# Performance work log

Hardware: AMD Instinct MI355X
Metric: run time of the kernel (lower is better)

The kernel has to match this reference:

```python
import jax, jax.numpy as jnp
import numpy as np

V, D, S, L, H, R, W = 32000, 512, 1536, 4, 4, 32, 128
HFF = int(2.0 * D)
N = S + 1          # anchor node at index 0 + S tokens
K = W + 2          # anchor edge + (W+1) causal window edges
LN_EPS = 1e-5


def _layer_norm(x, g, b):
    m = jnp.mean(x, axis=-1, keepdims=True)
    v = jnp.mean((x - m) ** 2, axis=-1, keepdims=True)
    return (x - m) * jax.lax.rsqrt(v + LN_EPS) * g + b


def _neighbors():
    # windowed causal neighborhood: node i sees nodes i-W..i, plus anchor (node 0)
    pos = jnp.arange(N)
    offs = jnp.arange(-W, 1)                     # W+1 offsets
    idx_w = pos[:, None] + offs[None, :]         # [N, W+1]
    valid_w = idx_w >= 0
    idx_w = jnp.maximum(idx_w, 0)
    anchor_valid = (pos > W)[:, None]            # avoid double-counting anchor when already in window
    idx = jnp.concatenate([jnp.zeros((N, 1), idx_w.dtype), idx_w], axis=1)   # [N, K]
    mask = jnp.concatenate([anchor_valid, valid_w], axis=1)                  # [N, K]
    return idx, mask


def setup_inputs() -> dict:
    key = jax.random.key(0)
    ks = jax.random.split(key, 10)
    std = 0.02
    return {
        'input_ids': jax.random.randint(ks[0], (1, S), 0, V),
        'embed': jax.random.normal(ks[1], (V, D), jnp.float32) * std,
        'pos_emb': jax.random.normal(ks[2], (S, D), jnp.float32) * std,
        'ln_in_g': jnp.ones((D,), jnp.float32),
        'ln_in_b': jnp.zeros((D,), jnp.float32),
        'anchor_state': jnp.zeros((), jnp.float32),
        'anchor_val': jax.random.normal(ks[3], (D,), jnp.float32) * std,
        'state_w': jax.random.normal(ks[4], (D,), jnp.float32) * std,
        'state_b': jnp.zeros((), jnp.float32),
        'wq': jax.random.normal(ks[5], (L, H, D, R), jnp.float32) * std,
        'wk': jax.random.normal(ks[6], (L, H, D, R), jnp.float32) * std,
        'gate': jnp.full((L,), 0.1, jnp.float32),
        'ln_g': jnp.ones((L, D), jnp.float32),
        'ln_b': jnp.zeros((L, D), jnp.float32),
        'ffn_w1': jax.random.normal(ks[7], (L, D, HFF), jnp.float32) * std,
        'ffn_b1': jnp.zeros((L, HFF), jnp.float32),
        'ffn_w2': jax.random.normal(ks[8], (L, HFF, D), jnp.float32) * std,
        'ffn_b2': jnp.zeros((L, D), jnp.float32),
        'ln2_g': jnp.ones((L, D), jnp.float32),
        'ln2_b': jnp.zeros((L, D), jnp.float32),
    }


def reference(input_ids, embed, pos_emb, ln_in_g, ln_in_b, anchor_state, anchor_val,
              state_w, state_b, wq, wk, gate, ln_g, ln_b,
              ffn_w1, ffn_b1, ffn_w2, ffn_b2, ln2_g, ln2_b):
    B = input_ids.shape[0]
    # token embedding + learned position encoding + input norm
    tok = embed[input_ids] + pos_emb[None]                 # [B,S,D]
    tok = _layer_norm(tok, ln_in_g, ln_in_b)
    tok_state = tok @ state_w + state_b                    # [B,S] scalar state per node
    # prepend anchor node
    val = jnp.concatenate([jnp.broadcast_to(anchor_val, (B, 1, D)), tok], axis=1)       # [B,N,D]
    state = jnp.concatenate([jnp.broadcast_to(anchor_state, (B, 1)), tok_state], axis=1)  # [B,N]
    idx, mask = _neighbors()
    scale = 1.0 / np.sqrt(R)
    for l in range(L):
        # low-rank multi-head pairwise scores on windowed neighborhood
        q = jnp.einsum('bnd,hdr->bnhr', val, wq[l])
        k = jnp.einsum('bnd,hdr->bnhr', val, wk[l])
        kg = k[:, idx]                                     # [B,N,K,H,R] gather
        s = jnp.einsum('bnhr,bnkhr->bnkh', q, kg) * scale  # [B,N,K,H]
        # signed_smoothmax head aggregation
        hw = jax.nn.softmax(jnp.abs(s), axis=-1)
        a = jnp.sum(s * hw, axis=-1)                       # [B,N,K]
        # signed_abs_softmax edge compression over neighborhood
        absa = jnp.where(mask[None], jnp.abs(a), -jnp.inf)
        e = jnp.sign(a) * jax.nn.softmax(absa, axis=-1)    # masked entries -> 0 weight
        # state-weighted edges
        sg = state[:, idx]                                 # [B,N,K]
        e = e * sg
        val_g = val[:, idx]                                # [B,N,K,D]
        d_val = jnp.einsum('bnk,bnkd->bnd', e, val_g)
        d_state = jnp.sum(e, axis=-1)
        # gated residual + post-norm
        state = state + gate[l] * d_state
        val = val + gate[l] * d_val
        val = _layer_norm(val, ln_g[l], ln_b[l])
        # value feed-forward (pre-norm, residual scale 1.0)
        h = jax.nn.gelu(_layer_norm(val, ln2_g[l], ln2_b[l]) @ ffn_w1[l] + ffn_b1[l], approximate=False)
        val = val + h @ ffn_w2[l] + ffn_b2[l]
    return val
```

## Files before the change

### kernel.cpp

```cpp
#include <hip/hip_runtime.h>
#include <hip/hip_bf16.h>

namespace {

constexpr int D    = 512;
constexpr int S    = 1536;
constexpr int N    = S + 1;
constexpr int L    = 4;
constexpr int H    = 4;
constexpr int R    = 32;
constexpr int W    = 128;
constexpr int HFF  = 1024;
constexpr float EPS = 1e-5f;

constexpr int TB   = 4;
constexpr int NB4  = (N + TB - 1) / TB;
constexpr int SP   = 133;
constexpr int SPAD = 136;

typedef __attribute__((ext_vector_type(8))) short short8;
typedef __attribute__((ext_vector_type(4))) float floatx4;

__device__ inline ushort f2bf(float x){
  __hip_bfloat16 h = __float2bfloat16(x);
  return *reinterpret_cast<ushort*>(&h);
}
__device__ inline float bf2f(uint u){
  union { uint u; float f; } c; c.u = u << 16; return c.f;
}

__device__ inline float wave_sum(float v){
#pragma unroll
  for (int o = 32; o; o >>= 1) v += __shfl_xor(v, o, 64);
  return v;
}
__device__ inline float wave_max(float v){
#pragma unroll
  for (int o = 32; o; o >>= 1) v = fmaxf(v, __shfl_xor(v, o, 64));
  return v;
}
__device__ inline float block_sum(float v, float* scr){
  v = wave_sum(v);
  __syncthreads();
  if ((threadIdx.x & 63) == 0) scr[threadIdx.x >> 6] = v;
  __syncthreads();
  return scr[0] + scr[1] + scr[2] + scr[3];
}

__global__ __launch_bounds__(256) void pack_wqk_bf(const float* __restrict__ wq,
                                                   const float* __restrict__ wk,
                                                   ushort* __restrict__ out){
  int i = blockIdx.x * 256 + threadIdx.x;
  int d = i & 511;
  int c = (i >> 9) & 255;
  int l = i >> 17;
  int cc = c & 127;
  int h = cc >> 5, r = cc & 31;
  const float* src = (c < 128) ? wq : wk;
  out[i] = f2bf(src[((l * H + h) * D + d) * R + r]);
}

__global__ __launch_bounds__(256) void transpose_bf(const float* __restrict__ src,
                                                    ushort* __restrict__ dst,
                                                    int rows, int cols){
  __shared__ float tile[32][33];
  const float* s = src + (size_t)blockIdx.z * rows * cols;
  ushort* d = dst + (size_t)blockIdx.z * rows * cols;
  int c0 = blockIdx.x * 32, r0 = blockIdx.y * 32;
  int tx = threadIdx.x & 31, ty = threadIdx.x >> 5;
  for (int rr = ty; rr < 32; rr += 8)
    tile[rr][tx] = s[(size_t)(r0 + rr) * cols + c0 + tx];
  __syncthreads();
  for (int rr = ty; rr < 32; rr += 8)
    d[(size_t)(c0 + rr) * rows + r0 + tx] = f2bf(tile[tx][rr]);
}

__global__ __launch_bounds__(256) void embed_ln_kernel(
    const int* __restrict__ ids, const float* __restrict__ embed,
    const float* __restrict__ pos, const float* __restrict__ g,
    const float* __restrict__ b, const float* __restrict__ anchor_val,
    const float* __restrict__ anchor_state, const float* __restrict__ state_w,
    const float* __restrict__ state_b, float* __restrict__ val,
    ushort* __restrict__ valbf, float* __restrict__ state)
{
  __shared__ float scr[4];
  int n = blockIdx.x, t = threadIdx.x;
  if (n == 0){
    float a0 = anchor_val[t], a1 = anchor_val[t + 256];
    val[t] = a0; val[t + 256] = a1;
    valbf[t] = f2bf(a0); valbf[t + 256] = f2bf(a1);
    if (t == 0) state[0] = anchor_state[0];
    return;
  }
  int tp = n - 1;
  int id = ids[tp];
  float x0 = embed[(size_t)id * D + t]       + pos[tp * D + t];
  float x1 = embed[(size_t)id * D + t + 256] + pos[tp * D + t + 256];
  float mean = block_sum(x0 + x1, scr) * (1.f / D);
  float var  = block_sum(x0 * x0 + x1 * x1, scr) * (1.f / D) - mean * mean;
  float rs   = rsqrtf(var + EPS);
  float y0 = (x0 - mean) * rs * g[t]       + b[t];
  float y1 = (x1 - mean) * rs * g[t + 256] + b[t + 256];
  val[n * D + t]       = y0;
  val[n * D + t + 256] = y1;
  valbf[n * D + t]       = f2bf(y0);
  valbf[n * D + t + 256] = f2bf(y1);
  float ts = block_sum(y0 * state_w[t] + y1 * state_w[t + 256], scr);
  if (t == 0) state[n] = ts + state_b[0];
}

template<int ACT>
__global__ __launch_bounds__(256) void gemm_bf16(
    const ushort* __restrict__ A, const ushort* __restrict__ Bt,
    const float* __restrict__ bias, const float* __restrict__ resid,
    float* __restrict__ C, ushort* __restrict__ Cbf,
    int M, int Kd, int Nc)
{
  constexpr int SLAB = 272;
  __shared__ ushort As[8 * SLAB];
  __shared__ ushort Bs[8 * SLAB];
  int row0 = blockIdx.y * 32;
  int col0 = blockIdx.x * 32;
  int t = threadIdx.x;
  int lane = t & 63, w = t >> 6;
  int wr = w & 1, wc = w >> 1;
  int q = lane >> 4, lm = lane & 15;

  int srow = t >> 3, skb = t & 7;
  int arow = min(row0 + srow, M - 1);
  const ushort* ag = A  + (size_t)arow * Kd + skb * 8;
  const ushort* bg = Bt + (size_t)(col0 + srow) * Kd + skb * 8;
  ushort* as = &As[skb * SLAB + srow * 8];
  ushort* bs = &Bs[skb * SLAB + srow * 8];

  const ushort* ar = &As[(wr * 16 + lm) * 8];
  const ushort* br = &Bs[(wc * 16 + lm) * 8];

  floatx4 acc = {0.f, 0.f, 0.f, 0.f};

  for (int k0 = 0; k0 < Kd; k0 += 64){
    uint4 av = *(const uint4*)(ag + k0);
    uint4 bv = *(const uint4*)(bg + k0);
    *(uint4*)as = av;
    *(uint4*)bs = bv;
    __syncthreads();
#pragma unroll
    for (int kk = 0; kk < 2; ++kk){
      short8 a = *(const short8*)(ar + (kk * 4 + q) * SLAB);
      short8 b = *(const short8*)(br + (kk * 4 + q) * SLAB);
      acc = __builtin_amdgcn_mfma_f32_16x16x32_bf16(a, b, acc, 0, 0, 0);
    }
    __syncthreads();
  }

  int col = col0 + wc * 16 + lm;
#pragma unroll
  for (int r = 0; r < 4; ++r){
    int row = row0 + wr * 16 + q * 4 + r;
    if (row >= M) continue;
    float v = acc[r] + (bias ? bias[col] : 0.f);
    if (ACT == 1) v = 0.5f * v * (1.f + erff(v * 0.70710678118654752f));
    if (resid) v += resid[(size_t)row * Nc + col];
    size_t o = (size_t)row * Nc + col;
    if (C)   C[o] = v;
    if (Cbf) Cbf[o] = f2bf(v);
  }
}

__global__ __launch_bounds__(256) void attn4_kernel(
    const ushort* __restrict__ qkbf, const float* __restrict__ val0,
    const ushort* __restrict__ val0bf, const float* __restrict__ state_in,
    float* __restrict__ val1, ushort* __restrict__ x2bf,
    float* __restrict__ state_out,
    const float* __restrict__ gate_p, const float* __restrict__ lng,
    const float* __restrict__ lnb, const float* __restrict__ ln2g,
    const float* __restrict__ ln2b)
{
  __shared__ float kg[64 * SPAD];
  __shared__ float qsh[TB * 128];
  __shared__ float ssh[16 * SPAD];
  __shared__ float ash[TB * SPAD];
  const int n0 = blockIdx.x * TB;
  const int t = threadIdx.x;
  const int w = t >> 6, l = t & 63;
  const float gate = gate_p[0];
  const float scale = 0.17677669529663687f;

#pragma unroll
  for (int i = t; i < TB * 128; i += 256){
    int it = i >> 7, ch = i & 127;
    int gr = min(n0 + it, N - 1);
    qsh[i] = bf2f((uint)qkbf[(size_t)gr * 256 + ch]);
  }

  for (int half = 0; half < 2; ++half){
    for (int i = t; i < SP * 16; i += 256){
      int c = i >> 4, c4 = i & 15;
      int g = (c == 132) ? 0 : min(max(n0 - W + c, 0), N - 1);
      uint2 v = *(const uint2*)&qkbf[(size_t)g * 256 + 128 + half * 64 + c4 * 4];
      int ch = c4 * 4;
      kg[(ch + 0) * SPAD + c] = bf2f(v.x & 0xffffu);
      kg[(ch + 1) * SPAD + c] = bf2f(v.x >> 16);
      kg[(ch + 2) * SPAD + c] = bf2f(v.y & 0xffffu);
      kg[(ch + 3) * SPAD + c] = bf2f(v.y >> 16);
    }
    __syncthreads();
    for (int tk = t; tk < TB * 2 * SP; tk += 256){
      int c = tk % SP;
      int th = tk / SP;
      int tok = th & 3, hh = th >> 2;
      int h = half * 2 + hh;
      const float* qs = &qsh[tok * 128 + h * 32];
      const float* ks = &kg[hh * 32 * SPAD + c];
      float acc = 0.f;
#pragma unroll
      for (int r = 0; r < 32; ++r) acc += qs[r] * ks[r * SPAD];
      ssh[(tok * 4 + h) * SPAD + c] = acc * scale;
    }
    __syncthreads();
  }

  for (int i = t; i < TB * SP; i += 256){
    int tok = i / SP, c = i - tok * SP;
    const float* sr = &ssh[tok * 4 * SPAD + c];
    float s0 = sr[0], s1 = sr[SPAD], s2 = sr[2 * SPAD], s3 = sr[3 * SPAD];
    float a0 = fabsf(s0), a1 = fabsf(s1), a2 = fabsf(s2), a3 = fabsf(s3);
    float m = fmaxf(fmaxf(a0, a1), fmaxf(a2, a3));
    float w0 = expf(a0 - m), w1 = expf(a1 - m), w2 = expf(a2 - m), w3 = expf(a3 - m);
    ash[tok * SPAD + c] = (s0 * w0 + s1 * w1 + s2 * w2 + s3 * w3) / (w0 + w1 + w2 + w3);
  }
  __syncthreads();

  {
    const int n = n0 + w;
    float* arow = &ash[w * SPAD];
    float a0 = arow[l];
    float a1 = arow[64 + l];
    float a2 = (l < 5) ? arow[128 + l] : 0.f;
    bool ok0 = (l >= w) && (n0 - W + l >= 0);
    bool ok1 = (n0 - W + 64 + l >= 0);
    bool ok2;
    if (l < 4)       ok2 = (l <= w);
    else if (l == 4) ok2 = (n > W);
    else             ok2 = false;
    float cand = -3.4e38f;
    if (ok0) cand = fabsf(a0);
    if (ok1) cand = fmaxf(cand, fabsf(a1));
    if (ok2) cand = fmaxf(cand, fabsf(a2));
    float m = wave_max(cand);
    float e0 = ok0 ? expf(fabsf(a0) - m) : 0.f;
    float e1 = ok1 ? expf(fabsf(a1) - m) : 0.f;
    float e2 = ok2 ? expf(fabsf(a2) - m) : 0.f;
    float inv = 1.f / wave_sum(e0 + e1 + e2);
    int g0 = min(max(n0 - W + l, 0), N - 1);
    int g1 = min(max(n0 - W + 64 + l, 0), N - 1);
    int g2 = (l < 4) ? min(n0 + l, N - 1) : 0;
    float sg0 = (a0 > 0.f) ? 1.f : ((a0 < 0.f) ? -1.f : 0.f);
    float sg1 = (a1 > 0.f) ? 1.f : ((a1 < 0.f) ? -1.f : 0.f);
    float sg2 = (a2 > 0.f) ? 1.f : ((a2 < 0.f) ? -1.f : 0.f);
    float t0 = sg0 * e0 * inv * state_in[g0];
    float t1 = sg1 * e1 * inv * state_in[g1];
    float t2 = (l < 5) ? sg2 * e2 * inv * state_in[g2] : 0.f;
    arow[l] = t0;
    arow[64 + l] = t1;
    if (l < 5) arow[128 + l] = t2;
    float ds = wave_sum(t0 + t1 + t2);
    if (l == 0 && n < N) state_out[n] = state_in[n] + gate * ds;
  }
  __syncthreads();

  float acc[TB][2];
#pragma unroll
  for (int k = 0; k < TB; ++k){ acc[k][0] = 0.f; acc[k][1] = 0.f; }
  {
    const int d0 = 2 * t;
    for (int c = 0; c < SP; ++c){
      int g = (c == 132) ? 0 : min(max(n0 - W + c, 0), N - 1);
      uint v = *(const uint*)&val0bf[(size_t)g * D + d0];
      float vx = bf2f(v & 0xffffu), vy = bf2f(v >> 16);
#pragma unroll
      for (int k = 0; k < TB; ++k){
        float e = ash[k * SPAD + c];
        acc[k][0] += e * vx;
        acc[k][1] += e * vy;
      }
    }
  }
  float* xbuf = kg;
  {
    const int d0 = 2 * t;
#pragma unroll
    for (int k = 0; k < TB; ++k){
      int nc = min(n0 + k, N - 1);
      float2 vv = *(const float2*)&val0[(size_t)nc * D + d0];
      xbuf[k * 520 + d0]     = vv.x + gate * acc[k][0];
      xbuf[k * 520 + d0 + 1] = vv.y + gate * acc[k][1];
    }
  }
  __syncthreads();

  {
    const int n = n0 + w;
    const int d = l * 8;
    const float* xr = &xbuf[w * 520 + d];
    float x[8];
#pragma unroll
    for (int j = 0; j < 8; ++j) x[j] = xr[j];
    float s1 = 0.f, s2 = 0.f;
#pragma unroll
    for (int j = 0; j < 8; ++j){ s1 += x[j]; s2 += x[j] * x[j]; }
    s1 = wave_sum(s1); s2 = wave_sum(s2);
    float mean = s1 * (1.f / D);
    float var  = s2 * (1.f / D) - mean * mean;
    float rs   = rsqrtf(var + EPS);
    float y[8];
    float u1 = 0.f, u2 = 0.f;
#pragma unroll
    for (int j = 0; j < 8; ++j){
      float yv = (x[j] - mean) * rs * lng[d + j] + lnb[d + j];
      y[j] = yv; u1 += yv; u2 += yv * yv;
    }
    u1 = wave_sum(u1); u2 = wave_sum(u2);
    float mean2 = u1 * (1.f / D);
    float var2  = u2 * (1.f / D) - mean2 * mean2;
    float rs2   = rsqrtf(var2 + EPS);
    if (n < N){
      *(float4*)&val1[(size_t)n * D + d]     = make_float4(y[0], y[1], y[2], y[3]);
      *(float4*)&val1[(size_t)n * D + d + 4] = make_float4(y[4], y[5], y[6], y[7]);
      uint4 pk;
      uint z0 = f2bf((y[0] - mean2) * rs2 * ln2g[d + 0] + ln2b[d + 0]);
      uint z1 = f2bf((y[1] - mean2) * rs2 * ln2g[d + 1] + ln2b[d + 1]);
      uint z2 = f2bf((y[2] - mean2) * rs2 * ln2g[d + 2] + ln2b[d + 2]);
      uint z3 = f2bf((y[3] - mean2) * rs2 * ln2g[d + 3] + ln2b[d + 3]);
      uint z4 = f2bf((y[4] - mean2) * rs2 * ln2g[d + 4] + ln2b[d + 4]);
      uint z5 = f2bf((y[5] - mean2) * rs2 * ln2g[d + 5] + ln2b[d + 5]);
      uint z6 = f2bf((y[6] - mean2) * rs2 * ln2g[d + 6] + ln2b[d + 6]);
      uint z7 = f2bf((y[7] - mean2) * rs2 * ln2g[d + 7] + ln2b[d + 7]);
      pk.x = z0 | (z1 << 16); pk.y = z2 | (z3 << 16);
      pk.z = z4 | (z5 << 16); pk.w = z6 | (z7 << 16);
      *(uint4*)&x2bf[(size_t)n * D + d] = pk;
    }
  }
}

}

extern "C" void kernel_launch(void* const* d_in, const int* in_sizes, int n_in,
                              void* d_out, int out_size, void* d_ws, size_t ws_size,
                              hipStream_t stream)
{
  (void)in_sizes; (void)n_in; (void)out_size; (void)ws_size;
  const int*   ids          = (const int*)d_in[0];
  const float* embed        = (const float*)d_in[1];
  const float* pos_emb      = (const float*)d_in[2];
  const float* ln_in_g      = (const float*)d_in[3];
  const float* ln_in_b      = (const float*)d_in[4];
  const float* anchor_state = (const float*)d_in[5];
  const float* anchor_val   = (const float*)d_in[6];
  const float* state_w      = (const float*)d_in[7];
  const float* state_b      = (const float*)d_in[8];
  const float* wq           = (const float*)d_in[9];
  const float* wk           = (const float*)d_in[10];
  const float* gate         = (const float*)d_in[11];
  const float* ln_g         = (const float*)d_in[12];
  const float* ln_b         = (const float*)d_in[13];
  const float* ffn_w1       = (const float*)d_in[14];
  const float* ffn_b1       = (const float*)d_in[15];
  const float* ffn_w2       = (const float*)d_in[16];
  const float* ffn_b2       = (const float*)d_in[17];
  const float* ln2_g        = (const float*)d_in[18];
  const float* ln2_b        = (const float*)d_in[19];
  float* out = (float*)d_out;

  float* wsf  = (float*)d_ws;
  float* val0 = wsf;  wsf += (size_t)N * D;
  float* val1 = wsf;  wsf += (size_t)N * D;
  ushort* wsu   = (ushort*)wsf;
  ushort* val0bf = wsu;  wsu += (size_t)N * D;
  ushort* x2bf   = wsu;  wsu += (size_t)N * D;
  ushort* hbf    = wsu;  wsu += (size_t)N * HFF;
  ushort* qkbf   = wsu;  wsu += (size_t)N * 256;
  ushort* wqkbf  = wsu;  wsu += (size_t)L * 256 * D;
  ushort* w1t    = wsu;  wsu += (size_t)L * HFF * D;
  ushort* w2t    = wsu;  wsu += (size_t)L * HFF * D;
  float* st0 = (float*)wsu;
  float* st1 = st0 + N;

  pack_wqk_bf<<<L * 512, 256, 0, stream>>>(wq, wk, wqkbf);
  transpose_bf<<<dim3(HFF / 32, D / 32, L), 256, 0, stream>>>(ffn_w1, w1t, D, HFF);
  transpose_bf<<<dim3(D / 32, HFF / 32, L), 256, 0, stream>>>(ffn_w2, w2t, HFF, D);
  embed_ln_kernel<<<N, 256, 0, stream>>>(ids, embed, pos_emb, ln_in_g, ln_in_b,
                                         anchor_val, anchor_state, state_w,
                                         state_b, val0, val0bf, st0);

  float* sin_  = st0;
  float* sout_ = st1;
  const int MT32 = (N + 31) / 32;
  for (int l = 0; l < L; ++l){
    gemm_bf16<0><<<dim3(256 / 32, MT32), 256, 0, stream>>>(
        val0bf, wqkbf + (size_t)l * 256 * D, nullptr, nullptr,
        nullptr, qkbf, N, D, 256);
    attn4_kernel<<<NB4, 256, 0, stream>>>(qkbf, val0, val0bf, sin_, val1, x2bf,
                                          sout_, gate + l, ln_g + l * D,
                                          ln_b + l * D, ln2_g + l * D,
                                          ln2_b + l * D);
    gemm_bf16<1><<<dim3(HFF / 32, MT32), 256, 0, stream>>>(
        x2bf, w1t + (size_t)l * HFF * D, ffn_b1 + l * HFF, nullptr,
        nullptr, hbf, N, D, HFF);
    float* dst = (l == L - 1) ? out : val0;
    gemm_bf16<0><<<dim3(D / 32, MT32), 256, 0, stream>>>(
        hbf, w2t + (size_t)l * HFF * D, ffn_b2 + l * D, val1,
        dst, val0bf, N, HFF, D);
    float* tmp = sin_; sin_ = sout_; sout_ = tmp;
  }
}
```

Measured before the change: 370.7 us.

## Merge all stages into one persistent kernel with software grid barriers

All separate launches (weight pack, transposes, embedding, and the per-layer GEMMs and attention) are replaced by a single persistent kernel of 512 blocks. Each stage loops over its tiles grid-stride, and stages are separated by a hierarchical atomic grid barrier. The aim is to remove launch overhead and inter-kernel gaps across about 19 launches. In exchange it adds barrier spin cost and relies on all 512 blocks being co-resident, which could deadlock or time out if occupancy falls short, and it limits tile parallelism to 512 blocks per stage.

```diff
diff --git a/kernel.cpp b/kernel.cpp
--- a/kernel.cpp
+++ b/kernel.cpp
@@ -1,5 +1,6 @@
 #include <hip/hip_runtime.h>
 #include <hip/hip_bf16.h>
+#include <stdint.h>
 
 namespace {
 
@@ -18,6 +19,11 @@
 constexpr int SP   = 133;
 constexpr int SPAD = 136;
 
+constexpr int GS   = 512;
+constexpr int SLAB = 272;
+
+constexpr int SM_BYTES = (64 * SPAD + TB * 128 + 16 * SPAD + TB * SPAD) * 4;
+
 typedef __attribute__((ext_vector_type(8))) short short8;
 typedef __attribute__((ext_vector_type(4))) float floatx4;
 
@@ -47,140 +53,184 @@
   return scr[0] + scr[1] + scr[2] + scr[3];
 }
 
-__global__ __launch_bounds__(256) void pack_wqk_bf(const float* __restrict__ wq,
-                                                   const float* __restrict__ wk,
-                                                   ushort* __restrict__ out){
-  int i = blockIdx.x * 256 + threadIdx.x;
-  int d = i & 511;
-  int c = (i >> 9) & 255;
-  int l = i >> 17;
-  int cc = c & 127;
-  int h = cc >> 5, r = cc & 31;
-  const float* src = (c < 128) ? wq : wk;
-  out[i] = f2bf(src[((l * H + h) * D + d) * R + r]);
-}
-
-__global__ __launch_bounds__(256) void transpose_bf(const float* __restrict__ src,
-                                                    ushort* __restrict__ dst,
-                                                    int rows, int cols){
-  __shared__ float tile[32][33];
-  const float* s = src + (size_t)blockIdx.z * rows * cols;
-  ushort* d = dst + (size_t)blockIdx.z * rows * cols;
-  int c0 = blockIdx.x * 32, r0 = blockIdx.y * 32;
-  int tx = threadIdx.x & 31, ty = threadIdx.x >> 5;
-  for (int rr = ty; rr < 32; rr += 8)
-    tile[rr][tx] = s[(size_t)(r0 + rr) * cols + c0 + tx];
-  __syncthreads();
-  for (int rr = ty; rr < 32; rr += 8)
-    d[(size_t)(c0 + rr) * rows + r0 + tx] = f2bf(tile[tx][rr]);
-}
-
-__global__ __launch_bounds__(256) void embed_ln_kernel(
+__device__ inline void grid_bar(uint* bar, uint gen){
+  __syncthreads();
+  if (threadIdx.x == 0){
+    __threadfence();
+    uint* slot = bar + ((blockIdx.x & 15) << 4);
+    uint prev = __hip_atomic_fetch_add(slot, 1u, __ATOMIC_ACQ_REL,
+                                       __HIP_MEMORY_SCOPE_AGENT);
+    if (prev + 1u == gen * (uint)(GS / 16)){
+      __hip_atomic_fetch_add(bar + 256, 1u, __ATOMIC_ACQ_REL,
+                             __HIP_MEMORY_SCOPE_AGENT);
+    }
+    const uint tgt = gen * 16u;
+    for (long it = 0; it < 10000000L; ++it){
+      if (__hip_atomic_load(bar + 256, __ATOMIC_RELAXED,
+                            __HIP_MEMORY_SCOPE_AGENT) >= tgt) break;
+      __builtin_amdgcn_s_sleep(1);
+    }
+    __threadfence();
+  }
+  __syncthreads();
+}
+
+static __device__ __forceinline__ void embed_phase(
     const int* __restrict__ ids, const float* __restrict__ embed,
     const float* __restrict__ pos, const float* __restrict__ g,
     const float* __restrict__ b, const float* __restrict__ anchor_val,
     const float* __restrict__ anchor_state, const float* __restrict__ state_w,
     const float* __restrict__ state_b, float* __restrict__ val,
-    ushort* __restrict__ valbf, float* __restrict__ state)
-{
-  __shared__ float scr[4];
-  int n = blockIdx.x, t = threadIdx.x;
-  if (n == 0){
-    float a0 = anchor_val[t], a1 = anchor_val[t + 256];
-    val[t] = a0; val[t + 256] = a1;
-    valbf[t] = f2bf(a0); valbf[t + 256] = f2bf(a1);
-    if (t == 0) state[0] = anchor_state[0];
-    return;
-  }
-  int tp = n - 1;
-  int id = ids[tp];
-  float x0 = embed[(size_t)id * D + t]       + pos[tp * D + t];
-  float x1 = embed[(size_t)id * D + t + 256] + pos[tp * D + t + 256];
-  float mean = block_sum(x0 + x1, scr) * (1.f / D);
-  float var  = block_sum(x0 * x0 + x1 * x1, scr) * (1.f / D) - mean * mean;
-  float rs   = rsqrtf(var + EPS);
-  float y0 = (x0 - mean) * rs * g[t]       + b[t];
-  float y1 = (x1 - mean) * rs * g[t + 256] + b[t + 256];
-  val[n * D + t]       = y0;
-  val[n * D + t + 256] = y1;
-  valbf[n * D + t]       = f2bf(y0);
-  valbf[n * D + t + 256] = f2bf(y1);
-  float ts = block_sum(y0 * state_w[t] + y1 * state_w[t + 256], scr);
-  if (t == 0) state[n] = ts + state_b[0];
+    ushort* __restrict__ valbf, float* __restrict__ state, char* SMbase)
+{
+  float* scr = (float*)SMbase;
+  const int t = threadIdx.x;
+  for (int n = blockIdx.x; n < N; n += GS){
+    if (n == 0){
+      float a0 = anchor_val[t], a1 = anchor_val[t + 256];
+      val[t] = a0; val[t + 256] = a1;
+      valbf[t] = f2bf(a0); valbf[t + 256] = f2bf(a1);
+      if (t == 0) state[0] = anchor_state[0];
+      continue;
+    }
+    int tp = n - 1;
+    int id = ids[tp];
+    float x0 = embed[(size_t)id * D + t]       + pos[tp * D + t];
+    float x1 = embed[(size_t)id * D + t + 256] + pos[tp * D + t + 256];
+    float mean = block_sum(x0 + x1, scr) * (1.f / D);
+    float var  = block_sum(x0 * x0 + x1 * x1, scr) * (1.f / D) - mean * mean;
+    float rs   = rsqrtf(var + EPS);
+    float y0 = (x0 - mean) * rs * g[t]       + b[t];
+    float y1 = (x1 - mean) * rs * g[t + 256] + b[t + 256];
+    val[n * D + t]       = y0;
+    val[n * D + t + 256] = y1;
+    valbf[n * D + t]       = f2bf(y0);
+    valbf[n * D + t + 256] = f2bf(y1);
+    float ts = block_sum(y0 * state_w[t] + y1 * state_w[t + 256], scr);
+    if (t == 0) state[n] = ts + state_b[0];
+  }
+}
+
+static __device__ __forceinline__ void pack_phase(
+    const float* __restrict__ wq, const float* __restrict__ wk,
+    ushort* __restrict__ out)
+{
+  for (int i = blockIdx.x * 256 + threadIdx.x; i < L * 256 * D; i += GS * 256){
+    int d = i & 511;
+    int c = (i >> 9) & 255;
+    int l = i >> 17;
+    int cc = c & 127;
+    int h = cc >> 5, r = cc & 31;
+    const float* src = (c < 128) ? wq : wk;
+    out[i] = f2bf(src[((l * H + h) * D + d) * R + r]);
+  }
+}
+
+static __device__ __forceinline__ void transpose_phase(
+    const float* __restrict__ ffn_w1, const float* __restrict__ ffn_w2,
+    ushort* __restrict__ w1t, ushort* __restrict__ w2t, char* SMbase)
+{
+  float* tile = (float*)SMbase;
+  const int t = threadIdx.x;
+  const int tx = t & 31, ty = t >> 5;
+  for (int tl = blockIdx.x; tl < 2 * L * 512; tl += GS){
+    const float* s; ushort* dd; int rows, cols, c0, r0;
+    if (tl < 2048){
+      int ll = tl >> 9, i = tl & 511;
+      rows = D; cols = HFF;
+      s  = ffn_w1 + (size_t)ll * D * HFF;
+      dd = w1t   + (size_t)ll * D * HFF;
+      c0 = (i & 31) << 5; r0 = (i >> 5) << 5;
+    } else {
+      int tl2 = tl - 2048;
+      int ll = tl2 >> 9, i = tl2 & 511;
+      rows = HFF; cols = D;
+      s  = ffn_w2 + (size_t)ll * D * HFF;
+      dd = w2t   + (size_t)ll * D * HFF;
+      c0 = (i & 15) << 5; r0 = (i >> 4) << 5;
+    }
+    __syncthreads();
+    for (int rr = ty; rr < 32; rr += 8)
+      tile[rr * 33 + tx] = s[(size_t)(r0 + rr) * cols + c0 + tx];
+    __syncthreads();
+    for (int rr = ty; rr < 32; rr += 8)
+      dd[(size_t)(c0 + rr) * rows + r0 + tx] = f2bf(tile[tx * 33 + rr]);
+  }
 }
 
 template<int ACT>
-__global__ __launch_bounds__(256) void gemm_bf16(
+static __device__ __forceinline__ void gemm_phase(
     const ushort* __restrict__ A, const ushort* __restrict__ Bt,
     const float* __restrict__ bias, const float* __restrict__ resid,
     float* __restrict__ C, ushort* __restrict__ Cbf,
-    int M, int Kd, int Nc)
-{
-  constexpr int SLAB = 272;
-  __shared__ ushort As[8 * SLAB];
-  __shared__ ushort Bs[8 * SLAB];
-  int row0 = blockIdx.y * 32;
-  int col0 = blockIdx.x * 32;
-  int t = threadIdx.x;
-  int lane = t & 63, w = t >> 6;
-  int wr = w & 1, wc = w >> 1;
-  int q = lane >> 4, lm = lane & 15;
-
-  int srow = t >> 3, skb = t & 7;
-  int arow = min(row0 + srow, M - 1);
-  const ushort* ag = A  + (size_t)arow * Kd + skb * 8;
-  const ushort* bg = Bt + (size_t)(col0 + srow) * Kd + skb * 8;
-  ushort* as = &As[skb * SLAB + srow * 8];
-  ushort* bs = &Bs[skb * SLAB + srow * 8];
-
-  const ushort* ar = &As[(wr * 16 + lm) * 8];
-  const ushort* br = &Bs[(wc * 16 + lm) * 8];
-
-  floatx4 acc = {0.f, 0.f, 0.f, 0.f};
-
-  for (int k0 = 0; k0 < Kd; k0 += 64){
-    uint4 av = *(const uint4*)(ag + k0);
-    uint4 bv = *(const uint4*)(bg + k0);
-    *(uint4*)as = av;
-    *(uint4*)bs = bv;
-    __syncthreads();
-#pragma unroll
-    for (int kk = 0; kk < 2; ++kk){
-      short8 a = *(const short8*)(ar + (kk * 4 + q) * SLAB);
-      short8 b = *(const short8*)(br + (kk * 4 + q) * SLAB);
-      acc = __builtin_amdgcn_mfma_f32_16x16x32_bf16(a, b, acc, 0, 0, 0);
-    }
-    __syncthreads();
-  }
-
-  int col = col0 + wc * 16 + lm;
-#pragma unroll
-  for (int r = 0; r < 4; ++r){
-    int row = row0 + wr * 16 + q * 4 + r;
-    if (row >= M) continue;
-    float v = acc[r] + (bias ? bias[col] : 0.f);
-    if (ACT == 1) v = 0.5f * v * (1.f + erff(v * 0.70710678118654752f));
-    if (resid) v += resid[(size_t)row * Nc + col];
-    size_t o = (size_t)row * Nc + col;
-    if (C)   C[o] = v;
-    if (Cbf) Cbf[o] = f2bf(v);
-  }
-}
-
-__global__ __launch_bounds__(256) void attn4_kernel(
-    const ushort* __restrict__ qkbf, const float* __restrict__ val0,
+    int M, int Kd, int Nc, char* SMbase)
+{
+  ushort* As = (ushort*)SMbase;
+  ushort* Bs = As + 8 * SLAB;
+  const int t = threadIdx.x;
+  const int lane = t & 63, w = t >> 6;
+  const int wr = w & 1, wc = w >> 1;
+  const int q = lane >> 4, lm = lane & 15;
+  const int srow = t >> 3, skb = t & 7;
+  const int ntx = Nc >> 5, nty = (M + 31) >> 5;
+  const int ntot = ntx * nty;
+
+  for (int tile = blockIdx.x; tile < ntot; tile += GS){
+    int row0 = (tile / ntx) << 5;
+    int col0 = (tile % ntx) << 5;
+    int arow = min(row0 + srow, M - 1);
+    const ushort* ag = A  + (size_t)arow * Kd + skb * 8;
+    const ushort* bg = Bt + (size_t)(col0 + srow) * Kd + skb * 8;
+    ushort* as = &As[skb * SLAB + srow * 8];
+    ushort* bs = &Bs[skb * SLAB + srow * 8];
+    const ushort* ar = &As[(wr * 16 + lm) * 8];
+    const ushort* br = &Bs[(wc * 16 + lm) * 8];
+
+    floatx4 acc = {0.f, 0.f, 0.f, 0.f};
+    for (int k0 = 0; k0 < Kd; k0 += 64){
+      uint4 av = *(const uint4*)(ag + k0);
+      uint4 bv = *(const uint4*)(bg + k0);
+      *(uint4*)as = av;
+      *(uint4*)bs = bv;
+      __syncthreads();
+#pragma unroll
+      for (int kk = 0; kk < 2; ++kk){
+        short8 a = *(const short8*)(ar + (kk * 4 + q) * SLAB);
+        short8 b = *(const short8*)(br + (kk * 4 + q) * SLAB);
+        acc = __builtin_amdgcn_mfma_f32_16x16x32_bf16(a, b, acc, 0, 0, 0);
+      }
+      __syncthreads();
+    }
+
+    int col = col0 + wc * 16 + lm;
+#pragma unroll
+    for (int r = 0; r < 4; ++r){
+      int row = row0 + wr * 16 + q * 4 + r;
+      if (row >= M) continue;
+      float v = acc[r] + (bias ? bias[col] : 0.f);
+      if (ACT == 1) v = 0.5f * v * (1.f + erff(v * 0.70710678118654752f));
+      if (resid) v += resid[(size_t)row * Nc + col];
+      size_t o = (size_t)row * Nc + col;
+      if (C)   C[o] = v;
+      if (Cbf) Cbf[o] = f2bf(v);
+    }
+  }
+}
+
+static __device__ __forceinline__ void attn_phase(
+    int blk, const ushort* __restrict__ qkbf, const float* __restrict__ val0,
     const ushort* __restrict__ val0bf, const float* __restrict__ state_in,
     float* __restrict__ val1, ushort* __restrict__ x2bf,
-    float* __restrict__ state_out,
-    const float* __restrict__ gate_p, const float* __restrict__ lng,
-    const float* __restrict__ lnb, const float* __restrict__ ln2g,
-    const float* __restrict__ ln2b)
-{
-  __shared__ float kg[64 * SPAD];
-  __shared__ float qsh[TB * 128];
-  __shared__ float ssh[16 * SPAD];
-  __shared__ float ash[TB * SPAD];
-  const int n0 = blockIdx.x * TB;
+    float* __restrict__ state_out, const float* __restrict__ gate_p,
+    const float* __restrict__ lng, const float* __restrict__ lnb,
+    const float* __restrict__ ln2g, const float* __restrict__ ln2b,
+    char* SMbase)
+{
+  float* kg  = (float*)SMbase;
+  float* qsh = kg + 64 * SPAD;
+  float* ssh = qsh + TB * 128;
+  float* ash = ssh + 16 * SPAD;
+  const int n0 = blk * TB;
   const int t = threadIdx.x;
   const int w = t >> 6, l = t & 63;
   const float gate = gate_p[0];
@@ -343,6 +393,63 @@
   }
 }
 
+__global__ void init_bar_kernel(uint* bar){
+  bar[threadIdx.x] = 0u;
+}
+
+__global__ __launch_bounds__(256, 2) void mega_kernel(
+    const int* __restrict__ ids, const float* __restrict__ embed,
+    const float* __restrict__ pos_emb, const float* __restrict__ ln_in_g,
+    const float* __restrict__ ln_in_b, const float* __restrict__ anchor_state,
+    const float* __restrict__ anchor_val, const float* __restrict__ state_w,
+    const float* __restrict__ state_b, const float* __restrict__ wq,
+    const float* __restrict__ wk, const float* __restrict__ gate,
+    const float* __restrict__ ln_g, const float* __restrict__ ln_b,
+    const float* __restrict__ ffn_w1, const float* __restrict__ ffn_b1,
+    const float* __restrict__ ffn_w2, const float* __restrict__ ffn_b2,
+    const float* __restrict__ ln2_g, const float* __restrict__ ln2_b,
+    float* __restrict__ out,
+    float* __restrict__ val0, float* __restrict__ val1,
+    ushort* __restrict__ val0bf, ushort* __restrict__ x2bf,
+    ushort* __restrict__ hbf, ushort* __restrict__ qkbf,
+    ushort* __restrict__ wqkbf, ushort* __restrict__ w1t,
+    ushort* __restrict__ w2t, float* __restrict__ st0,
+    float* __restrict__ st1, uint* __restrict__ bar)
+{
+  __shared__ __align__(16) char SM[SM_BYTES];
+  uint gen = 0;
+
+  embed_phase(ids, embed, pos_emb, ln_in_g, ln_in_b, anchor_val, anchor_state,
+              state_w, state_b, val0, val0bf, st0, SM);
+  pack_phase(wq, wk, wqkbf);
+  transpose_phase(ffn_w1, ffn_w2, w1t, w2t, SM);
+  grid_bar(bar, ++gen);
+
+  float* sin_  = st0;
+  float* sout_ = st1;
+  for (int l = 0; l < L; ++l){
+    gemm_phase<0>(val0bf, wqkbf + (size_t)l * 256 * D, nullptr, nullptr,
+                  nullptr, qkbf, N, D, 256, SM);
+    grid_bar(bar, ++gen);
+
+    for (int blk = blockIdx.x; blk < NB4; blk += GS)
+      attn_phase(blk, qkbf, val0, val0bf, sin_, val1, x2bf, sout_, gate + l,
+                 ln_g + l * D, ln_b + l * D, ln2_g + l * D, ln2_b + l * D, SM);
+    grid_bar(bar, ++gen);
+
+    gemm_phase<1>(x2bf, w1t + (size_t)l * HFF * D, ffn_b1 + l * HFF, nullptr,
+                  nullptr, hbf, N, D, HFF, SM);
+    grid_bar(bar, ++gen);
+
+    float* dst = (l == L - 1) ? out : val0;
+    gemm_phase<0>(hbf, w2t + (size_t)l * HFF * D, ffn_b2 + l * D, val1,
+                  dst, val0bf, N, HFF, D, SM);
+    if (l != L - 1) grid_bar(bar, ++gen);
+
+    float* tmp = sin_; sin_ = sout_; sout_ = tmp;
+  }
+}
+
 }
 
 extern "C" void kernel_launch(void* const* d_in, const int* in_sizes, int n_in,
@@ -385,32 +492,14 @@
   ushort* w2t    = wsu;  wsu += (size_t)L * HFF * D;
   float* st0 = (float*)wsu;
   float* st1 = st0 + N;
-
-  pack_wqk_bf<<<L * 512, 256, 0, stream>>>(wq, wk, wqkbf);
-  transpose_bf<<<dim3(HFF / 32, D / 32, L), 256, 0, stream>>>(ffn_w1, w1t, D, HFF);
-  transpose_bf<<<dim3(D / 32, HFF / 32, L), 256, 0, stream>>>(ffn_w2, w2t, HFF, D);
-  embed_ln_kernel<<<N, 256, 0, stream>>>(ids, embed, pos_emb, ln_in_g, ln_in_b,
-                                         anchor_val, anchor_state, state_w,
-                                         state_b, val0, val0bf, st0);
-
-  float* sin_  = st0;
-  float* sout_ = st1;
-  const int MT32 = (N + 31) / 32;
-  for (int l = 0; l < L; ++l){
-    gemm_bf16<0><<<dim3(256 / 32, MT32), 256, 0, stream>>>(
-        val0bf, wqkbf + (size_t)l * 256 * D, nullptr, nullptr,
-        nullptr, qkbf, N, D, 256);
-    attn4_kernel<<<NB4, 256, 0, stream>>>(qkbf, val0, val0bf, sin_, val1, x2bf,
-                                          sout_, gate + l, ln_g + l * D,
-                                          ln_b + l * D, ln2_g + l * D,
-                                          ln2_b + l * D);
-    gemm_bf16<1><<<dim3(HFF / 32, MT32), 256, 0, stream>>>(
-        x2bf, w1t + (size_t)l * HFF * D, ffn_b1 + l * HFF, nullptr,
-        nullptr, hbf, N, D, HFF);
-    float* dst = (l == L - 1) ? out : val0;
-    gemm_bf16<0><<<dim3(D / 32, MT32), 256, 0, stream>>>(
-        hbf, w2t + (size_t)l * HFF * D, ffn_b2 + l * D, val1,
-        dst, val0bf, N, HFF, D);
-    float* tmp = sin_; sin_ = sout_; sout_ = tmp;
-  }
-}
+  uintptr_t pb = (uintptr_t)(st1 + N);
+  pb = (pb + 255) & ~(uintptr_t)255;
+  uint* bar = (uint*)pb;
+
+  init_bar_kernel<<<1, 512, 0, stream>>>(bar);
+  mega_kernel<<<GS, 256, 0, stream>>>(
+      ids, embed, pos_emb, ln_in_g, ln_in_b, anchor_state, anchor_val,
+      state_w, state_b, wq, wk, gate, ln_g, ln_b, ffn_w1, ffn_b1,
+      ffn_w2, ffn_b2, ln2_g, ln2_b, out,
+      val0, val1, val0bf, x2bf, hbf, qkbf, wqkbf, w1t, w2t, st0, st1, bar);
+}
```

Result: slower. 947.5 us (+155.6%).
